# Performance work log

Measured on AMD Instinct MI355X. Metric: run time of the kernel, lower is better.

The kernel has to match this reference:

```python
import jax, jax.numpy as jnp
import numpy as np

EMBED_DIM = 768
N_HEADS = 12
MLP_HID = 3072  # mlp_ratio 4.0
LN_EPS = 1e-6


def setup_inputs() -> dict:
    key = jax.random.key(0)
    ks = jax.random.split(key, 12)
    B, N, C = 4, 2048, EMBED_DIM
    s = 0.02
    return {
        "x": jax.random.normal(ks[0], (B, N, C), jnp.float32),
        "mask": jnp.ones((B, N), jnp.int32),
        "ln1_g": jnp.ones((C,), jnp.float32),
        "ln1_b": jnp.zeros((C,), jnp.float32),
        "qkv_w": jax.random.normal(ks[1], (C, 3 * C), jnp.float32) * s,
        "qkv_b": jnp.zeros((3 * C,), jnp.float32),
        "proj_w": jax.random.normal(ks[2], (C, C), jnp.float32) * s,
        "proj_b": jnp.zeros((C,), jnp.float32),
        "ln2_g": jnp.ones((C,), jnp.float32),
        "ln2_b": jnp.zeros((C,), jnp.float32),
        "fc1_w": jax.random.normal(ks[3], (C, MLP_HID), jnp.float32) * s,
        "fc1_b": jnp.zeros((MLP_HID,), jnp.float32),
        "fc2_w": jax.random.normal(ks[4], (MLP_HID, C), jnp.float32) * s,
        "fc2_b": jnp.zeros((C,), jnp.float32),
    }


def _layernorm(x, g, b):
    mu = jnp.mean(x, axis=-1, keepdims=True)
    var = jnp.mean(jnp.square(x - mu), axis=-1, keepdims=True)
    return (x - mu) * jax.lax.rsqrt(var + LN_EPS) * g + b


def _block(x, mask, ln1_g, ln1_b, qkv_w, qkv_b, proj_w, proj_b,
           ln2_g, ln2_b, fc1_w, fc1_b, fc2_w, fc2_b):
    B, N, C = x.shape
    H, D = N_HEADS, C // N_HEADS
    scale = D ** -0.5

    # --- attention (pre-norm) ---
    h = _layernorm(x, ln1_g, ln1_b)
    qkv = h @ qkv_w + qkv_b                      # [B,N,3C]
    qkv = qkv.reshape(B, N, 3, H, D).transpose(2, 0, 3, 1, 4)
    q, k, v = qkv[0], qkv[1], qkv[2]             # [B,H,N,D]
    scores = jnp.einsum("bhqd,bhkd->bhqk", q, k * scale)
    # 2-D mask path: (bsz, seq) -> (bsz, 1, seq, 1), mask queries
    m = mask[:, None, :, None]
    scores = jnp.where(m == 0, jnp.finfo(scores.dtype).min, scores)
    attn = jax.nn.softmax(scores, axis=-1)
    vals = jnp.einsum("bhqk,bhkd->bhqd", attn, v)
    vals = vals.transpose(0, 2, 1, 3).reshape(B, N, C)
    x = x + (vals @ proj_w + proj_b)

    # --- MLP (pre-norm, GELU exact) ---
    h = _layernorm(x, ln2_g, ln2_b)
    h = jax.nn.gelu(h @ fc1_w + fc1_b, approximate=False)
    x = x + (h @ fc2_w + fc2_b)
    return x


def reference(x, mask, ln1_g, ln1_b, qkv_w, qkv_b, proj_w, proj_b,
              ln2_g, ln2_b, fc1_w, fc1_b, fc2_w, fc2_b):
    return _block(x, mask, ln1_g, ln1_b, qkv_w, qkv_b, proj_w, proj_b,
                  ln2_g, ln2_b, fc1_w, fc1_b, fc2_w, fc2_b)
```

## Files before the change

### kernel.cpp

```cpp
#include <hip/hip_runtime.h>
#include <hip/hip_bf16.h>
#include <math.h>

using bf16 = __hip_bfloat16;
typedef short s16x8 __attribute__((ext_vector_type(8)));
typedef float f32x4 __attribute__((ext_vector_type(4)));
typedef float f32x16 __attribute__((ext_vector_type(16)));

#define LOG2E 1.4426950408889634f

__device__ inline unsigned short f2bf(float f) {
    bf16 h = __float2bfloat16(f);
    return __builtin_bit_cast(unsigned short, h);
}

__device__ inline void gload_lds16(const void* g, void* l) {
    __builtin_amdgcn_global_load_lds(
        (const __attribute__((address_space(1))) void*)g,
        (__attribute__((address_space(3))) void*)l, 16, 0, 0);
}

__device__ inline float swap_halves(float x, int hi) {
    unsigned a = __builtin_bit_cast(unsigned, x);
    unsigned b = a;
    asm volatile("v_permlane32_swap_b32 %0, %1" : "+v"(a), "+v"(b));
    return hi ? __builtin_bit_cast(float, a) : __builtin_bit_cast(float, b);
}

__device__ inline unsigned cvtpk(float lo, float hi) {
    unsigned r;
    asm("v_cvt_pk_bf16_f32 %0, %1, %2" : "=v"(r) : "v"(lo), "v"(hi));
    return r;
}

__device__ inline s16x8 build_pfrag(float p0, float p1, float p2, float p3,
                                    float p4, float p5, float p6, float p7) {
    unsigned w01 = cvtpk(p0, p1);
    unsigned w23 = cvtpk(p2, p3);
    unsigned w45 = cvtpk(p4, p5);
    unsigned w67 = cvtpk(p6, p7);
    asm volatile("v_permlane32_swap_b32 %0, %1" : "+v"(w01), "+v"(w45));
    asm volatile("v_permlane32_swap_b32 %0, %1" : "+v"(w23), "+v"(w67));
    int4 t = {(int)w01, (int)w23, (int)w45, (int)w67};
    return __builtin_bit_cast(s16x8, t);
}

__global__ __launch_bounds__(256) void transpose_bf16(
    const float* __restrict__ in, bf16* __restrict__ out, int K, int N)
{
    __shared__ float tile[32][33];
    const int bx = blockIdx.x * 32;
    const int by = blockIdx.y * 32;
    const int tx = threadIdx.x, ty = threadIdx.y;
    #pragma unroll
    for (int i = 0; i < 32; i += 8)
        tile[ty + i][tx] = in[(size_t)(by + ty + i) * N + bx + tx];
    __syncthreads();
    #pragma unroll
    for (int i = 0; i < 32; i += 8)
        out[(size_t)(bx + ty + i) * K + by + tx] = __float2bfloat16(tile[tx][ty + i]);
}

__global__ __launch_bounds__(256) void ln_kernel(
    const float* __restrict__ x, const float* __restrict__ g,
    const float* __restrict__ bb, bf16* __restrict__ out)
{
    const int row = blockIdx.x;
    const float* xr = x + (size_t)row * 768;
    float v[3];
    float s = 0.f, s2 = 0.f;
    #pragma unroll
    for (int i = 0; i < 3; ++i) {
        v[i] = xr[threadIdx.x + i * 256];
        s += v[i];
        s2 += v[i] * v[i];
    }
    #pragma unroll
    for (int off = 1; off < 64; off <<= 1) {
        s += __shfl_xor(s, off);
        s2 += __shfl_xor(s2, off);
    }
    __shared__ float rs[4], rs2[4];
    const int wave = threadIdx.x >> 6;
    if ((threadIdx.x & 63) == 0) { rs[wave] = s; rs2[wave] = s2; }
    __syncthreads();
    s = rs[0] + rs[1] + rs[2] + rs[3];
    s2 = rs2[0] + rs2[1] + rs2[2] + rs2[3];
    const float mu = s * (1.f / 768.f);
    const float var = s2 * (1.f / 768.f) - mu * mu;
    const float r = rsqrtf(var + 1e-6f);
    bf16* orow = out + (size_t)row * 768;
    #pragma unroll
    for (int i = 0; i < 3; ++i) {
        const int col = threadIdx.x + i * 256;
        orow[col] = __float2bfloat16((v[i] - mu) * r * g[col] + bb[col]);
    }
}

#define BM 128
#define BN 128
#define BK 64

template <int EPI>
__global__ __launch_bounds__(256) void gemm_bt(
    const bf16* __restrict__ A, const bf16* __restrict__ Bt,
    const float* __restrict__ bias, const float* __restrict__ resid,
    void* __restrict__ outp, const int* __restrict__ mask,
    bf16* __restrict__ Qb, bf16* __restrict__ Kb, bf16* __restrict__ Vt,
    int M, int N, int K)
{
    __shared__ alignas(16) char As[BM * BK * 2];
    __shared__ alignas(16) char Bs[BN * BK * 2];
    const int tid = threadIdx.x;
    const int lane = tid & 63;
    const int wave = tid >> 6;
    const int wm = wave >> 1, wn = wave & 1;
    const int lr = lane & 15, lg = lane >> 4;
    const int bm = blockIdx.x, bn = blockIdx.y;

    f32x4 acc[4][4] = {};

    const size_t a_row0 = (size_t)bm * BM;
    const size_t b_row0 = (size_t)bn * BN;

    for (int kt = 0; kt < K; kt += BK) {
        #pragma unroll
        for (int i = 0; i < 4; ++i) {
            const int id = tid + i * 256;
            const int row = id >> 3, c = id & 7;
            const int cs = (c ^ (row & 7)) * 8;
            gload_lds16(A + (a_row0 + row) * K + kt + cs, As + id * 16);
            gload_lds16(Bt + (b_row0 + row) * K + kt + cs, Bs + id * 16);
        }
        __syncthreads();
        #pragma unroll
        for (int ks = 0; ks < 2; ++ks) {
            s16x8 af[4], bfr[4];
            #pragma unroll
            for (int mf = 0; mf < 4; ++mf) {
                const int row = wm * 64 + mf * 16 + lr;
                const int c = ks * 4 + lg;
                af[mf] = *reinterpret_cast<const s16x8*>(As + row * 128 + ((c ^ (row & 7)) * 16));
            }
            #pragma unroll
            for (int nf = 0; nf < 4; ++nf) {
                const int row = wn * 64 + nf * 16 + lr;
                const int c = ks * 4 + lg;
                bfr[nf] = *reinterpret_cast<const s16x8*>(Bs + row * 128 + ((c ^ (row & 7)) * 16));
            }
            #pragma unroll
            for (int mf = 0; mf < 4; ++mf)
                #pragma unroll
                for (int nf = 0; nf < 4; ++nf)
                    acc[mf][nf] = __builtin_amdgcn_mfma_f32_16x16x32_bf16(
                        af[mf], bfr[nf], acc[mf][nf], 0, 0, 0);
        }
        __syncthreads();
    }

    if (EPI == 3) {
        const int rq = bn / 6;
        const int bb_ = bm >> 4;
        const int cb = bn * 128 - rq * 768 + wn * 64;
        if (rq == 2) {
            #pragma unroll
            for (int nf = 0; nf < 4; ++nf) {
                const int c = cb + nf * 16 + lr;
                const int h = c >> 6, d = c & 63;
                const size_t base = ((size_t)(bb_ * 12 + h) * 64 + d) * 2048;
                const int gn = bn * 128 + wn * 64 + nf * 16 + lr;
                const float bs = bias[gn];
                #pragma unroll
                for (int mf = 0; mf < 4; ++mf) {
                    unsigned short pk[4];
                    #pragma unroll
                    for (int i = 0; i < 4; ++i) pk[i] = f2bf(acc[mf][nf][i] + bs);
                    const int n = (bm * 128 + wm * 64 + mf * 16 + 4 * lg) & 2047;
                    *reinterpret_cast<int2*>(Vt + base + n) =
                        *reinterpret_cast<const int2*>(pk);
                }
            }
        } else {
            bf16* dst = (rq == 0) ? Qb : Kb;
            #pragma unroll
            for (int mf = 0; mf < 4; ++mf) {
                #pragma unroll
                for (int i = 0; i < 4; ++i) {
                    const int gm = bm * 128 + wm * 64 + mf * 16 + 4 * lg + i;
                    const int n = gm & 2047;
                    const float msc = (rq == 0) ? (mask[gm] ? 0.125f : 0.f) : 1.f;
                    #pragma unroll
                    for (int nf = 0; nf < 4; ++nf) {
                        const int c = cb + nf * 16 + lr;
                        const int h = c >> 6, d = c & 63;
                        const int gn = bn * 128 + wn * 64 + nf * 16 + lr;
                        const float v = (acc[mf][nf][i] + bias[gn]) * msc;
                        dst[((size_t)(bb_ * 12 + h) * 2048 + n) * 64 + d] =
                            __float2bfloat16(v);
                    }
                }
            }
        }
        return;
    }

    #pragma unroll
    for (int mf = 0; mf < 4; ++mf) {
        #pragma unroll
        for (int i = 0; i < 4; ++i) {
            const int gm = bm * BM + wm * 64 + mf * 16 + 4 * lg + i;
            #pragma unroll
            for (int nf = 0; nf < 4; ++nf) {
                const int gn = bn * BN + wn * 64 + nf * 16 + lr;
                float v = acc[mf][nf][i] + bias[gn];
                if (EPI == 1) v += resid[(size_t)gm * N + gn];
                if (EPI == 2) v = 0.5f * v * (1.0f + erff(v * 0.70710678118654752f));
                if (EPI == 1)
                    reinterpret_cast<float*>(outp)[(size_t)gm * N + gn] = v;
                else
                    reinterpret_cast<bf16*>(outp)[(size_t)gm * N + gn] = __float2bfloat16(v);
            }
        }
    }
}

__global__ __launch_bounds__(256, 3) void attn_kernel(
    const bf16* __restrict__ Qb, const bf16* __restrict__ Kb,
    const bf16* __restrict__ Vt, bf16* __restrict__ out)
{
    __shared__ alignas(16) char Ks[2][64 * 128];
    __shared__ alignas(16) char Vs[2][64 * 128];

    const int lin = blockIdx.x;
    const int xcd = lin & 7, slot = lin >> 3;
    const int pair = xcd * 6 + (slot >> 4);
    const int qb = slot & 15;
    const int b = pair / 12, h = pair % 12;

    const int tid = threadIdx.x, lane = tid & 63, wave = tid >> 6;
    const int lq = lane & 31;
    const int hi = lane >> 5;
    const size_t bh = (size_t)(b * 12 + h);
    const bf16* Kh = Kb + bh * 2048 * 64;
    const bf16* Vh = Vt + bh * 64 * 2048;
    const int q0w = qb * 128 + wave * 32;

    s16x8 qf[4];
    {
        const bf16* qp = Qb + (bh * 2048 + q0w + lq) * 64 + 8 * hi;
        #pragma unroll
        for (int ks = 0; ks < 4; ++ks)
            qf[ks] = *reinterpret_cast<const s16x8*>(qp + 16 * ks);
    }

    float m_r = -1e30f, l_r = 0.f;
    f32x16 o0 = {}, o1 = {};

    #define STAGE(buf, kb)                                                        \
        do {                                                                      \
            _Pragma("unroll")                                                     \
            for (int i_ = 0; i_ < 2; ++i_) {                                      \
                const int id_ = tid + i_ * 256;                                   \
                const int row_ = id_ >> 3, c_ = id_ & 7;                          \
                const int cs_ = (c_ ^ (row_ & 7)) * 8;                            \
                gload_lds16(Kh + (size_t)((kb) * 64 + row_) * 64 + cs_,           \
                            Ks[buf] + id_ * 16);                                  \
                gload_lds16(Vh + (size_t)row_ * 2048 + (kb) * 64 + cs_,           \
                            Vs[buf] + id_ * 16);                                  \
            }                                                                     \
        } while (0)

    STAGE(0, 0);
    __syncthreads();
    int cur = 0;

    for (int kb = 0; kb < 32; ++kb) {
        if (kb < 31) STAGE(cur ^ 1, kb + 1);
        const char* Kc = Ks[cur];
        const char* Vc = Vs[cur];

        f32x16 st0 = {}, st1 = {};
        __builtin_amdgcn_s_setprio(1);
        #pragma unroll
        for (int ks = 0; ks < 4; ++ks) {
            const int row = lq;
            const int c8 = 2 * ks + hi;
            const s16x8 kf = *reinterpret_cast<const s16x8*>(
                Kc + row * 128 + ((c8 ^ (row & 7)) * 16));
            st0 = __builtin_amdgcn_mfma_f32_32x32x16_bf16(kf, qf[ks], st0, 0, 0, 0);
        }
        #pragma unroll
        for (int ks = 0; ks < 4; ++ks) {
            const int row = 32 + lq;
            const int c8 = 2 * ks + hi;
            const s16x8 kf = *reinterpret_cast<const s16x8*>(
                Kc + row * 128 + ((c8 ^ (row & 7)) * 16));
            st1 = __builtin_amdgcn_mfma_f32_32x32x16_bf16(kf, qf[ks], st1, 0, 0, 0);
        }
        __builtin_amdgcn_s_setprio(0);

        float mxa = fmaxf(st0[0], st0[1]), mxb = fmaxf(st1[0], st1[1]);
        #pragma unroll
        for (int r = 2; r < 16; r += 2) {
            mxa = fmaxf(mxa, fmaxf(st0[r], st0[r + 1]));
            mxb = fmaxf(mxb, fmaxf(st1[r], st1[r + 1]));
        }
        float mx = fmaxf(mxa, mxb);
        mx = fmaxf(mx, swap_halves(mx, hi));
        const float ml = mx * LOG2E;
        if (!__all(ml - m_r <= 8.0f)) {
            const float mnew = fmaxf(m_r, ml);
            const float alpha = __builtin_amdgcn_exp2f(m_r - mnew);
            m_r = mnew;
            l_r *= alpha;
            #pragma unroll
            for (int r = 0; r < 16; ++r) { o0[r] *= alpha; o1[r] *= alpha; }
        }
        float p0[16], p1[16];
        float rsa = 0.f, rsb = 0.f;
        #pragma unroll
        for (int r = 0; r < 16; ++r) {
            p0[r] = __builtin_amdgcn_exp2f(fmaf(st0[r], LOG2E, -m_r));
            p1[r] = __builtin_amdgcn_exp2f(fmaf(st1[r], LOG2E, -m_r));
            rsa += p0[r];
            rsb += p1[r];
        }
        float rs = rsa + rsb;
        rs += swap_halves(rs, hi);
        l_r += rs;

        const s16x8 pf00 = build_pfrag(p0[0], p0[1], p0[2], p0[3], p0[4], p0[5], p0[6], p0[7]);
        const s16x8 pf01 = build_pfrag(p0[8], p0[9], p0[10], p0[11], p0[12], p0[13], p0[14], p0[15]);
        const s16x8 pf10 = build_pfrag(p1[0], p1[1], p1[2], p1[3], p1[4], p1[5], p1[6], p1[7]);
        const s16x8 pf11 = build_pfrag(p1[8], p1[9], p1[10], p1[11], p1[12], p1[13], p1[14], p1[15]);

        __builtin_amdgcn_s_setprio(1);
        #pragma unroll
        for (int kf4 = 0; kf4 < 4; ++kf4) {
            const s16x8 pf = (kf4 == 0) ? pf00 : (kf4 == 1) ? pf01
                           : (kf4 == 2) ? pf10 : pf11;
            const int c8 = 2 * kf4 + hi;
            {
                const int row = lq;
                const s16x8 vf = *reinterpret_cast<const s16x8*>(
                    Vc + row * 128 + ((c8 ^ (row & 7)) * 16));
                o0 = __builtin_amdgcn_mfma_f32_32x32x16_bf16(vf, pf, o0, 0, 0, 0);
            }
            {
                const int row = 32 + lq;
                const s16x8 vf = *reinterpret_cast<const s16x8*>(
                    Vc + row * 128 + ((c8 ^ (row & 7)) * 16));
                o1 = __builtin_amdgcn_mfma_f32_32x32x16_bf16(vf, pf, o1, 0, 0, 0);
            }
        }
        __builtin_amdgcn_s_setprio(0);

        __syncthreads();
        cur ^= 1;
    }
    #undef STAGE

    const float rl = 1.0f / l_r;
    bf16* orow = out + (size_t)(b * 2048 + q0w + lq) * 768 + h * 64;
    #pragma unroll
    for (int g = 0; g < 4; ++g) {
        unsigned short pk0[4], pk1[4];
        #pragma unroll
        for (int i = 0; i < 4; ++i) {
            pk0[i] = f2bf(o0[4 * g + i] * rl);
            pk1[i] = f2bf(o1[4 * g + i] * rl);
        }
        const int d0 = 8 * g + 4 * hi;
        *reinterpret_cast<int2*>(orow + d0) = *reinterpret_cast<const int2*>(pk0);
        *reinterpret_cast<int2*>(orow + 32 + d0) = *reinterpret_cast<const int2*>(pk1);
    }
}

extern "C" void kernel_launch(void* const* d_in, const int* in_sizes, int n_in,
                              void* d_out, int out_size, void* d_ws, size_t ws_size,
                              hipStream_t stream)
{
    (void)in_sizes; (void)n_in; (void)out_size; (void)ws_size;
    const float* x      = (const float*)d_in[0];
    const int*   mask   = (const int*)d_in[1];
    const float* ln1_g  = (const float*)d_in[2];
    const float* ln1_b  = (const float*)d_in[3];
    const float* qkv_w  = (const float*)d_in[4];
    const float* qkv_b  = (const float*)d_in[5];
    const float* proj_w = (const float*)d_in[6];
    const float* proj_b = (const float*)d_in[7];
    const float* ln2_g  = (const float*)d_in[8];
    const float* ln2_b  = (const float*)d_in[9];
    const float* fc1_w  = (const float*)d_in[10];
    const float* fc1_b  = (const float*)d_in[11];
    const float* fc2_w  = (const float*)d_in[12];
    const float* fc2_b  = (const float*)d_in[13];
    float* out = (float*)d_out;
    char* ws = (char*)d_ws;

    bf16*  Wt_qkv  = (bf16*)(ws + 0);
    bf16*  Wt_proj = (bf16*)(ws + 3538944);
    bf16*  Wt_fc1  = (bf16*)(ws + 4718592);
    bf16*  Wt_fc2  = (bf16*)(ws + 9437184);
    bf16*  hbuf    = (bf16*)(ws + 14155776);
    bf16*  attnout = (bf16*)(ws + 64487424);
    float* x1      = (float*)(ws + 77070336);
    bf16*  h2      = (bf16*)(ws + 102236160);
    bf16*  a1      = (bf16*)(ws + 114819072);
    bf16*  Qb      = (bf16*)(ws + 114819072);
    bf16*  Kb      = (bf16*)(ws + 127401984);
    bf16*  Vt      = (bf16*)(ws + 139984896);

    const dim3 tb(32, 8);
    transpose_bf16<<<dim3(2304 / 32, 768 / 32), tb, 0, stream>>>(qkv_w, Wt_qkv, 768, 2304);
    transpose_bf16<<<dim3(768 / 32, 768 / 32), tb, 0, stream>>>(proj_w, Wt_proj, 768, 768);
    transpose_bf16<<<dim3(3072 / 32, 768 / 32), tb, 0, stream>>>(fc1_w, Wt_fc1, 768, 3072);
    transpose_bf16<<<dim3(768 / 32, 3072 / 32), tb, 0, stream>>>(fc2_w, Wt_fc2, 3072, 768);

    ln_kernel<<<8192, 256, 0, stream>>>(x, ln1_g, ln1_b, hbuf);
    gemm_bt<3><<<dim3(64, 18), 256, 0, stream>>>(hbuf, Wt_qkv, qkv_b, nullptr, nullptr,
                                                 mask, Qb, Kb, Vt, 8192, 2304, 768);
    attn_kernel<<<768, 256, 0, stream>>>(Qb, Kb, Vt, attnout);
    gemm_bt<1><<<dim3(64, 6), 256, 0, stream>>>(attnout, Wt_proj, proj_b, x, x1,
                                                nullptr, nullptr, nullptr, nullptr, 8192, 768, 768);
    ln_kernel<<<8192, 256, 0, stream>>>(x1, ln2_g, ln2_b, h2);
    gemm_bt<2><<<dim3(64, 24), 256, 0, stream>>>(h2, Wt_fc1, fc1_b, nullptr, a1,
                                                 nullptr, nullptr, nullptr, nullptr, 8192, 3072, 768);
    gemm_bt<1><<<dim3(64, 6), 256, 0, stream>>>(a1, Wt_fc2, fc2_b, x1, out,
                                                nullptr, nullptr, nullptr, nullptr, 8192, 768, 3072);
}
```

Measured before the change: 288.5 us.

## Coalesce V-transpose stores via LDS, approximate GELU, restructure attention LDS layout

The QKV epilogue for V now stages the tile in shared memory and writes transposed rows with 16-byte coalesced stores instead of scattered 8-byte writes. The exact erf GELU is replaced by a tanh-form approximation built from exp2 and rcp, which is cheaper but slightly changes numerics. The attention kernel precomputes its K/V staging offsets and uses a new swizzled LDS layout, so fragment reads reduce to a base pointer plus a small XOR offset. The row-max reduction uses three-input max chains.

```diff
diff --git a/kernel.cpp b/kernel.cpp
--- a/kernel.cpp
+++ b/kernel.cpp
@@ -12,6 +12,10 @@
 __device__ inline unsigned short f2bf(float f) {
     bf16 h = __float2bfloat16(f);
     return __builtin_bit_cast(unsigned short, h);
+}
+
+__device__ inline float max3f(float a, float b, float c) {
+    return fmaxf(fmaxf(a, b), c);
 }
 
 __device__ inline void gload_lds16(const void* g, void* l) {
@@ -109,8 +113,9 @@
     bf16* __restrict__ Qb, bf16* __restrict__ Kb, bf16* __restrict__ Vt,
     int M, int N, int K)
 {
-    __shared__ alignas(16) char As[BM * BK * 2];
-    __shared__ alignas(16) char Bs[BN * BK * 2];
+    __shared__ alignas(16) char smem[32768];
+    char* As = smem;
+    char* Bs = smem + 16384;
     const int tid = threadIdx.x;
     const int lane = tid & 63;
     const int wave = tid >> 6;
@@ -161,13 +166,11 @@
     if (EPI == 3) {
         const int rq = bn / 6;
         const int bb_ = bm >> 4;
-        const int cb = bn * 128 - rq * 768 + wn * 64;
         if (rq == 2) {
+            char* Ws = smem + wave * 8192;
             #pragma unroll
             for (int nf = 0; nf < 4; ++nf) {
-                const int c = cb + nf * 16 + lr;
-                const int h = c >> 6, d = c & 63;
-                const size_t base = ((size_t)(bb_ * 12 + h) * 64 + d) * 2048;
+                const int cl = nf * 16 + lr;
                 const int gn = bn * 128 + wn * 64 + nf * 16 + lr;
                 const float bs = bias[gn];
                 #pragma unroll
@@ -175,12 +178,27 @@
                     unsigned short pk[4];
                     #pragma unroll
                     for (int i = 0; i < 4; ++i) pk[i] = f2bf(acc[mf][nf][i] + bs);
-                    const int n = (bm * 128 + wm * 64 + mf * 16 + 4 * lg) & 2047;
-                    *reinterpret_cast<int2*>(Vt + base + n) =
-                        *reinterpret_cast<const int2*>(pk);
+                    const int slot = (2 * mf + (lg >> 1)) ^ (cl & 7);
+                    *reinterpret_cast<long long*>(Ws + cl * 128 + slot * 16 + (lg & 1) * 8) =
+                        *reinterpret_cast<const long long*>(pk);
                 }
             }
+            __syncthreads();
+            const int nb = (bm * 128 + wm * 64) & 2047;
+            const int cb = (bn - 12) * 128 + wn * 64;
+            #pragma unroll
+            for (int r = 0; r < 8; ++r) {
+                const int cl = r * 8 + (lane >> 3);
+                const int j = lane & 7;
+                const int4 vv = *reinterpret_cast<const int4*>(
+                    Ws + cl * 128 + ((j ^ (cl & 7)) * 16));
+                const int c = cb + cl;
+                const int hh = c >> 6, dd = c & 63;
+                *reinterpret_cast<int4*>(
+                    Vt + ((size_t)(bb_ * 12 + hh) * 64 + dd) * 2048 + nb + j * 8) = vv;
+            }
         } else {
+            const int cb = bn * 128 - rq * 768 + wn * 64;
             bf16* dst = (rq == 0) ? Qb : Kb;
             #pragma unroll
             for (int mf = 0; mf < 4; ++mf) {
@@ -214,7 +232,12 @@
                 const int gn = bn * BN + wn * 64 + nf * 16 + lr;
                 float v = acc[mf][nf][i] + bias[gn];
                 if (EPI == 1) v += resid[(size_t)gm * N + gn];
-                if (EPI == 2) v = 0.5f * v * (1.0f + erff(v * 0.70710678118654752f));
+                if (EPI == 2) {
+                    const float x3 = v * v * v;
+                    const float z = fmaf(x3, 0.044715f, v) * 2.3022080f;
+                    const float e = __builtin_amdgcn_exp2f(z);
+                    v = v - v * __builtin_amdgcn_rcpf(1.f + e);
+                }
                 if (EPI == 1)
                     reinterpret_cast<float*>(outp)[(size_t)gm * N + gn] = v;
                 else
@@ -253,21 +276,38 @@
             qf[ks] = *reinterpret_cast<const s16x8*>(qp + 16 * ks);
     }
 
+    int sKoff0, sKoff1, dst0, dst1;
+    size_t sVoff0, sVoff1;
+    {
+        const int id0 = tid;
+        const int R0 = id0 >> 4;
+        const int u0 = (id0 & 15) ^ (R0 & 15);
+        const int rt0 = 2 * R0 + (u0 >> 3), s80 = (u0 & 7) * 8;
+        sKoff0 = rt0 * 64 + s80;
+        sVoff0 = (size_t)rt0 * 2048 + s80;
+        dst0 = id0 * 16;
+        const int id1 = tid + 256;
+        const int R1 = id1 >> 4;
+        const int u1 = (id1 & 15) ^ (R1 & 15);
+        const int rt1 = 2 * R1 + (u1 >> 3), s81 = (u1 & 7) * 8;
+        sKoff1 = rt1 * 64 + s81;
+        sVoff1 = (size_t)rt1 * 2048 + s81;
+        dst1 = id1 * 16;
+    }
+
+    const int rh = lq >> 1;
+    const int m7 = rh & 7;
+    const int rbase = rh * 256 + (((((lq & 1) << 3) ^ (rh & 8))) << 4);
+
     float m_r = -1e30f, l_r = 0.f;
     f32x16 o0 = {}, o1 = {};
 
-    #define STAGE(buf, kb)                                                        \
-        do {                                                                      \
-            _Pragma("unroll")                                                     \
-            for (int i_ = 0; i_ < 2; ++i_) {                                      \
-                const int id_ = tid + i_ * 256;                                   \
-                const int row_ = id_ >> 3, c_ = id_ & 7;                          \
-                const int cs_ = (c_ ^ (row_ & 7)) * 8;                            \
-                gload_lds16(Kh + (size_t)((kb) * 64 + row_) * 64 + cs_,           \
-                            Ks[buf] + id_ * 16);                                  \
-                gload_lds16(Vh + (size_t)row_ * 2048 + (kb) * 64 + cs_,           \
-                            Vs[buf] + id_ * 16);                                  \
-            }                                                                     \
+    #define STAGE(buf, kb)                                                    \
+        do {                                                                  \
+            gload_lds16(Kh + (kb) * 4096 + sKoff0, Ks[buf] + dst0);           \
+            gload_lds16(Vh + (kb) * 64 + sVoff0, Vs[buf] + dst0);             \
+            gload_lds16(Kh + (kb) * 4096 + sKoff1, Ks[buf] + dst1);           \
+            gload_lds16(Vh + (kb) * 64 + sVoff1, Vs[buf] + dst1);             \
         } while (0)
 
     STAGE(0, 0);
@@ -276,36 +316,36 @@
 
     for (int kb = 0; kb < 32; ++kb) {
         if (kb < 31) STAGE(cur ^ 1, kb + 1);
-        const char* Kc = Ks[cur];
-        const char* Vc = Vs[cur];
+        const char* Kc = Ks[cur] + rbase;
+        const char* Vc = Vs[cur] + rbase;
 
         f32x16 st0 = {}, st1 = {};
         __builtin_amdgcn_s_setprio(1);
         #pragma unroll
         for (int ks = 0; ks < 4; ++ks) {
-            const int row = lq;
-            const int c8 = 2 * ks + hi;
-            const s16x8 kf = *reinterpret_cast<const s16x8*>(
-                Kc + row * 128 + ((c8 ^ (row & 7)) * 16));
-            st0 = __builtin_amdgcn_mfma_f32_32x32x16_bf16(kf, qf[ks], st0, 0, 0, 0);
-        }
-        #pragma unroll
-        for (int ks = 0; ks < 4; ++ks) {
-            const int row = 32 + lq;
-            const int c8 = 2 * ks + hi;
-            const s16x8 kf = *reinterpret_cast<const s16x8*>(
-                Kc + row * 128 + ((c8 ^ (row & 7)) * 16));
-            st1 = __builtin_amdgcn_mfma_f32_32x32x16_bf16(kf, qf[ks], st1, 0, 0, 0);
+            const int so = (((2 * ks + hi) ^ m7) << 4);
+            const s16x8 kf0 = *reinterpret_cast<const s16x8*>(Kc + so);
+            st0 = __builtin_amdgcn_mfma_f32_32x32x16_bf16(kf0, qf[ks], st0, 0, 0, 0);
+            const s16x8 kf1 = *reinterpret_cast<const s16x8*>(Kc + 4096 + so);
+            st1 = __builtin_amdgcn_mfma_f32_32x32x16_bf16(kf1, qf[ks], st1, 0, 0, 0);
         }
         __builtin_amdgcn_s_setprio(0);
 
-        float mxa = fmaxf(st0[0], st0[1]), mxb = fmaxf(st1[0], st1[1]);
-        #pragma unroll
-        for (int r = 2; r < 16; r += 2) {
-            mxa = fmaxf(mxa, fmaxf(st0[r], st0[r + 1]));
-            mxb = fmaxf(mxb, fmaxf(st1[r], st1[r + 1]));
-        }
-        float mx = fmaxf(mxa, mxb);
+        float a0 = max3f(st0[0], st0[1], st0[2]);
+        float a1 = max3f(st0[3], st0[4], st0[5]);
+        float a2 = max3f(st0[6], st0[7], st0[8]);
+        float a3 = max3f(st0[9], st0[10], st0[11]);
+        float a4 = max3f(st0[12], st0[13], st0[14]);
+        float b0 = max3f(st1[0], st1[1], st1[2]);
+        float b1 = max3f(st1[3], st1[4], st1[5]);
+        float b2 = max3f(st1[6], st1[7], st1[8]);
+        float b3 = max3f(st1[9], st1[10], st1[11]);
+        float b4 = max3f(st1[12], st1[13], st1[14]);
+        a0 = max3f(a0, a1, a2);
+        a3 = max3f(a3, a4, st0[15]);
+        b0 = max3f(b0, b1, b2);
+        b3 = max3f(b3, b4, st1[15]);
+        float mx = fmaxf(fmaxf(a0, a3), fmaxf(b0, b3));
         mx = fmaxf(mx, swap_halves(mx, hi));
         const float ml = mx * LOG2E;
         if (!__all(ml - m_r <= 8.0f)) {
@@ -339,19 +379,11 @@
         for (int kf4 = 0; kf4 < 4; ++kf4) {
             const s16x8 pf = (kf4 == 0) ? pf00 : (kf4 == 1) ? pf01
                            : (kf4 == 2) ? pf10 : pf11;
-            const int c8 = 2 * kf4 + hi;
-            {
-                const int row = lq;
-                const s16x8 vf = *reinterpret_cast<const s16x8*>(
-                    Vc + row * 128 + ((c8 ^ (row & 7)) * 16));
-                o0 = __builtin_amdgcn_mfma_f32_32x32x16_bf16(vf, pf, o0, 0, 0, 0);
-            }
-            {
-                const int row = 32 + lq;
-                const s16x8 vf = *reinterpret_cast<const s16x8*>(
-                    Vc + row * 128 + ((c8 ^ (row & 7)) * 16));
-                o1 = __builtin_amdgcn_mfma_f32_32x32x16_bf16(vf, pf, o1, 0, 0, 0);
-            }
+            const int so = (((2 * kf4 + hi) ^ m7) << 4);
+            const s16x8 vf0 = *reinterpret_cast<const s16x8*>(Vc + so);
+            o0 = __builtin_amdgcn_mfma_f32_32x32x16_bf16(vf0, pf, o0, 0, 0, 0);
+            const s16x8 vf1 = *reinterpret_cast<const s16x8*>(Vc + 4096 + so);
+            o1 = __builtin_amdgcn_mfma_f32_32x32x16_bf16(vf1, pf, o1, 0, 0, 0);
         }
         __builtin_amdgcn_s_setprio(0);
 
```

After: 282.7 us. 2.0% less time.
